# Performance work log

Measured on AMD Instinct MI355X. Metric: run time of the kernel, lower is better.

The kernel has to match this reference:

```python
import jax, jax.numpy as jnp
import numpy as np

N_DRUG, N_TARGET, N_EDGES, H = 50000, 20000, 500000, 256


def setup_inputs() -> dict:
    key = jax.random.key(0)
    ks = jax.random.split(key, 6)
    s = 1.0 / np.sqrt(2 * H)
    return {
        "z_drug": jax.random.normal(ks[0], (N_DRUG, H), dtype=jnp.float32),
        "z_target": jax.random.normal(ks[1], (N_TARGET, H), dtype=jnp.float32),
        "row": jax.random.randint(ks[2], (N_EDGES,), 0, N_DRUG, dtype=jnp.int64),
        "col": jax.random.randint(ks[3], (N_EDGES,), 0, N_TARGET, dtype=jnp.int64),
        "W1": jax.random.normal(ks[4], (2 * H, H), dtype=jnp.float32) * s,
        "b1": jnp.zeros((H,), dtype=jnp.float32),
        "W2": jax.random.normal(ks[5], (H, 1), dtype=jnp.float32) * (1.0 / np.sqrt(H)),
        "b2": jnp.zeros((1,), dtype=jnp.float32),
    }


def reference(z_drug, z_target, row, col, W1, b1, W2, b2):
    # gather endpoint embeddings by edge index, concat -> [E, 2H]
    zc = jnp.concatenate([z_drug[row], z_target[col]], axis=-1)
    h = jax.nn.relu(zc @ W1 + b1)          # [E, H]
    return h @ W2 + b2                     # [E, 1]
```

## Files before the change

kernel.cpp:

```cpp
#include <hip/hip_runtime.h>
#include <hip/hip_bf16.h>
#include <stdint.h>


typedef unsigned short u16;
typedef __attribute__((ext_vector_type(8))) short short8;
typedef __attribute__((ext_vector_type(4))) float f32x4;

#define HDIM 256
#define KDIM 512
#define BM 128
#define BK 64
#define NWAVE 4

__device__ __forceinline__ u16 f2bf(float f) {
  union { float f; uint32_t u; } v; v.f = f;
  uint32_t u = v.u;
  return (u16)((u + 0x7fffu + ((u >> 16) & 1u)) >> 16);
}

__device__ __forceinline__ void gl2lds16(const void* g, void* l) {
  __builtin_amdgcn_global_load_lds(
      (const __attribute__((address_space(1))) unsigned int*)g,
      (__attribute__((address_space(3))) unsigned int*)l,
      16, 0, 0);
}

#define CVT_BLOCKS 4096
__global__ void prep_kernel(const float* __restrict__ zd_f,
                            const float* __restrict__ zt_f,
                            const float* __restrict__ w1,
                            u16* __restrict__ zdb, u16* __restrict__ ztb,
                            u16* __restrict__ w1t, int n4d, int n4t) {
  const int b = blockIdx.x;
  if (b < 32) {
    __shared__ float tile[64][65];
    const int k0 = (b >> 2) * 64, n0 = (b & 3) * 64;
    const int tx = threadIdx.x & 63, ty = threadIdx.x >> 6;
#pragma unroll
    for (int i = ty; i < 64; i += 4)
      tile[i][tx] = w1[(size_t)(k0 + i) * HDIM + n0 + tx];
    __syncthreads();
#pragma unroll
    for (int i = ty; i < 64; i += 4)
      w1t[(size_t)(n0 + i) * KDIM + k0 + tx] = f2bf(tile[tx][i]);
  } else {
    const int idx = (b - 32) * 256 + threadIdx.x;
    const int stride = CVT_BLOCKS * 256;
    for (int i = idx; i < n4d; i += stride) {
      float4 v = ((const float4*)zd_f)[i];
      ushort4 o; o.x = f2bf(v.x); o.y = f2bf(v.y); o.z = f2bf(v.z); o.w = f2bf(v.w);
      ((ushort4*)zdb)[i] = o;
    }
    for (int i = idx; i < n4t; i += stride) {
      float4 v = ((const float4*)zt_f)[i];
      ushort4 o; o.x = f2bf(v.x); o.y = f2bf(v.y); o.z = f2bf(v.z); o.w = f2bf(v.w);
      ((ushort4*)ztb)[i] = o;
    }
  }
}

__global__ __launch_bounds__(256, 2) void edge_mlp_kernel(
    const u16* __restrict__ zd, const u16* __restrict__ zt,
    const int* __restrict__ row, const int* __restrict__ col,
    const u16* __restrict__ w1t, const float* __restrict__ b1,
    const float* __restrict__ w2, const float* __restrict__ b2,
    float* __restrict__ out, int E) {
  __shared__ u16 lA[BM * BK];
  __shared__ u16 lB[HDIM * BK];
  __shared__ float lP[NWAVE * BM];

  const int tid  = threadIdx.x;
  const int wid  = tid >> 6;
  const int lane = tid & 63;
  const int e0   = blockIdx.x * BM;
  const int r8   = lane >> 3;
  const int slog = ((lane & 7) ^ (r8 & 7)) * 8;

  uint32_t offD[4], offT[4];
#pragma unroll
  for (int t = 0; t < 4; ++t) {
    int ge = min(e0 + wid * 32 + r8 + 8 * t, E - 1);
    offD[t] = (uint32_t)row[ge] * HDIM;
    offT[t] = (uint32_t)col[ge] * HDIM;
  }
  const u16* pB = w1t + (uint32_t)(wid * 64 + r8) * KDIM + slog;

  u16* lAw = &lA[(wid * 32) * BK];
  u16* lBw = &lB[(wid * 64) * BK];

  f32x4 acc[8][4];
#pragma unroll
  for (int i = 0; i < 8; ++i)
#pragma unroll
    for (int j = 0; j < 4; ++j) acc[i][j] = f32x4{0.f, 0.f, 0.f, 0.f};

  const int colid = lane & 15;
  const int quad  = lane >> 4;
  const int csw   = colid & 7;

  for (int kc = 0; kc < 8; ++kc) {
    const int koff = (kc & 3) * BK;
    const u16* zbase = (kc < 4) ? zd : zt;

    __syncthreads();
#pragma unroll
    for (int t = 0; t < 4; ++t) {
      uint32_t o = (kc < 4) ? offD[t] : offT[t];
      gl2lds16(zbase + o + koff + slog, lAw + (8 * t) * BK);
    }
#pragma unroll
    for (int j = 0; j < 8; ++j)
      gl2lds16(pB + (size_t)j * 8 * KDIM + kc * BK, lBw + j * 8 * BK);
    __syncthreads();

#pragma unroll
    for (int ks = 0; ks < BK; ks += 32) {
      const int sl = (ks >> 3) + quad;
      short8 aF[8], bF[4];
#pragma unroll
      for (int rt = 0; rt < 8; ++rt)
        aF[rt] = *(const short8*)&lA[(rt * 16 + colid) * BK + ((sl ^ csw) * 8)];
#pragma unroll
      for (int ct = 0; ct < 4; ++ct)
        bF[ct] = *(const short8*)&lB[(wid * 64 + ct * 16 + colid) * BK + ((sl ^ csw) * 8)];
#pragma unroll
      for (int rt = 0; rt < 8; ++rt)
#pragma unroll
        for (int ct = 0; ct < 4; ++ct)
          acc[rt][ct] = __builtin_amdgcn_mfma_f32_16x16x32_bf16(
              aF[rt], bF[ct], acc[rt][ct], 0, 0, 0);
    }
  }

  float b1v[4], w2v[4];
#pragma unroll
  for (int ct = 0; ct < 4; ++ct) {
    int n = wid * 64 + ct * 16 + colid;
    b1v[ct] = b1[n];
    w2v[ct] = w2[n];
  }
#pragma unroll
  for (int rt = 0; rt < 8; ++rt)
#pragma unroll
    for (int j = 0; j < 4; ++j) {
      float s = 0.f;
#pragma unroll
      for (int ct = 0; ct < 4; ++ct)
        s += fmaxf(acc[rt][ct][j] + b1v[ct], 0.f) * w2v[ct];
#pragma unroll
      for (int off = 8; off >= 1; off >>= 1)
        s += __shfl_xor(s, off, 16);
      if (colid == 0)
        lP[wid * BM + rt * 16 + quad * 4 + j] = s;
    }
  __syncthreads();
  if (tid < BM) {
    int ge = e0 + tid;
    if (ge < E)
      out[ge] = lP[tid] + lP[BM + tid] + lP[2 * BM + tid] + lP[3 * BM + tid]
                + b2[0];
  }
}

__global__ void fallback_kernel(
    const float* __restrict__ zd, const float* __restrict__ zt,
    const int* __restrict__ row, const int* __restrict__ col,
    const float* __restrict__ W1, const float* __restrict__ b1,
    const float* __restrict__ W2, const float* __restrict__ b2,
    float* __restrict__ out, int E) {
  __shared__ float zc[16][512];
  __shared__ float red[4][16];
  const int e0 = blockIdx.x * 16;
  const int tid = threadIdx.x;
  for (int i = tid; i < 16 * 512; i += 256) {
    int e = i >> 9, k = i & 511;
    int ge = min(e0 + e, E - 1);
    zc[e][k] = (k < HDIM) ? zd[(size_t)row[ge] * HDIM + k]
                          : zt[(size_t)col[ge] * HDIM + (k - HDIM)];
  }
  __syncthreads();
  float acc[16];
#pragma unroll
  for (int e = 0; e < 16; ++e) acc[e] = 0.f;
  for (int k = 0; k < KDIM; ++k) {
    float w = W1[k * HDIM + tid];
#pragma unroll
    for (int e = 0; e < 16; ++e) acc[e] += zc[e][k] * w;
  }
  float wv = W2[tid], bv = b1[tid];
  const int lane = tid & 63, wid = tid >> 6;
#pragma unroll
  for (int e = 0; e < 16; ++e) {
    float pv = fmaxf(acc[e] + bv, 0.f) * wv;
#pragma unroll
    for (int off = 32; off >= 1; off >>= 1) pv += __shfl_down(pv, off, 64);
    if (lane == 0) red[wid][e] = pv;
  }
  __syncthreads();
  if (tid < 16) {
    int ge = e0 + tid;
    if (ge < E)
      out[ge] = red[0][tid] + red[1][tid] + red[2][tid] + red[3][tid] + b2[0];
  }
}

extern "C" void kernel_launch(void* const* d_in, const int* in_sizes, int n_in,
                              void* d_out, int out_size, void* d_ws, size_t ws_size,
                              hipStream_t stream) {
  const float* zd_f = (const float*)d_in[0];
  const float* zt_f = (const float*)d_in[1];
  const int*   row  = (const int*)d_in[2];
  const int*   col  = (const int*)d_in[3];
  const float* W1   = (const float*)d_in[4];
  const float* b1   = (const float*)d_in[5];
  const float* W2   = (const float*)d_in[6];
  const float* b2   = (const float*)d_in[7];
  float* out = (float*)d_out;

  const int E  = in_sizes[2];
  const int ND = in_sizes[0] / HDIM;
  const int NT = in_sizes[1] / HDIM;

  size_t off_w1t = 0;
  size_t off_zd  = (size_t)KDIM * HDIM * sizeof(u16);
  size_t off_zt  = off_zd + (size_t)ND * HDIM * sizeof(u16);
  size_t need    = off_zt + (size_t)NT * HDIM * sizeof(u16);

  if (ws_size >= need) {
    u16* w1t = (u16*)((char*)d_ws + off_w1t);
    u16* zdb = (u16*)((char*)d_ws + off_zd);
    u16* ztb = (u16*)((char*)d_ws + off_zt);
    int n4d = ND * HDIM / 4, n4t = NT * HDIM / 4;
    prep_kernel<<<32 + CVT_BLOCKS, 256, 0, stream>>>(zd_f, zt_f, W1,
                                                     zdb, ztb, w1t, n4d, n4t);
    edge_mlp_kernel<<<(E + BM - 1) / BM, 256, 0, stream>>>(
        zdb, ztb, row, col, w1t, b1, W2, b2, out, E);
  } else {
    fallback_kernel<<<(E + 15) / 16, 256, 0, stream>>>(
        zd_f, zt_f, row, col, W1, b1, W2, b2, out, E);
  }
}
```

Before: 268.1 us.

## Load A fragments directly to registers and double-buffer W1 tiles in LDS

Each wave now owns 32 edges across all 256 hidden outputs instead of 128 edges by 64 outputs. The gathered embedding rows are read straight from global memory into MFMA register fragments, prefetched one K-chunk ahead. W1 tiles are double-buffered in LDS so the next chunk's load overlaps the current MFMAs, cutting one barrier per iteration. The final reduction no longer goes through LDS; the cost is more W1 reads per edge from LDS and direct global gathers that bypass LDS.

```diff
diff --git a/kernel.cpp b/kernel.cpp
--- a/kernel.cpp
+++ b/kernel.cpp
@@ -11,7 +11,7 @@
 #define KDIM 512
 #define BM 128
 #define BK 64
-#define NWAVE 4
+#define NKC 8
 
 __device__ __forceinline__ u16 f2bf(float f) {
   union { float f; uint32_t u; } v; v.f = f;
@@ -66,101 +66,105 @@
     const u16* __restrict__ w1t, const float* __restrict__ b1,
     const float* __restrict__ w2, const float* __restrict__ b2,
     float* __restrict__ out, int E) {
-  __shared__ u16 lA[BM * BK];
-  __shared__ u16 lB[HDIM * BK];
-  __shared__ float lP[NWAVE * BM];
-
-  const int tid  = threadIdx.x;
-  const int wid  = tid >> 6;
-  const int lane = tid & 63;
-  const int e0   = blockIdx.x * BM;
-  const int r8   = lane >> 3;
-  const int slog = ((lane & 7) ^ (r8 & 7)) * 8;
-
-  uint32_t offD[4], offT[4];
-#pragma unroll
-  for (int t = 0; t < 4; ++t) {
-    int ge = min(e0 + wid * 32 + r8 + 8 * t, E - 1);
-    offD[t] = (uint32_t)row[ge] * HDIM;
-    offT[t] = (uint32_t)col[ge] * HDIM;
-  }
-  const u16* pB = w1t + (uint32_t)(wid * 64 + r8) * KDIM + slog;
-
-  u16* lAw = &lA[(wid * 32) * BK];
-  u16* lBw = &lB[(wid * 64) * BK];
-
-  f32x4 acc[8][4];
-#pragma unroll
-  for (int i = 0; i < 8; ++i)
-#pragma unroll
-    for (int j = 0; j < 4; ++j) acc[i][j] = f32x4{0.f, 0.f, 0.f, 0.f};
-
+  __shared__ u16 lB[2][HDIM * BK];
+
+  const int tid   = threadIdx.x;
+  const int wid   = tid >> 6;
+  const int lane  = tid & 63;
   const int colid = lane & 15;
   const int quad  = lane >> 4;
+  const int e0    = blockIdx.x * BM;
+  const int r8    = lane >> 3;
+  const int slog  = ((lane & 7) ^ (r8 & 7)) * 8;
   const int csw   = colid & 7;
 
-  for (int kc = 0; kc < 8; ++kc) {
-    const int koff = (kc & 3) * BK;
-    const u16* zbase = (kc < 4) ? zd : zt;
-
-    __syncthreads();
-#pragma unroll
-    for (int t = 0; t < 4; ++t) {
-      uint32_t o = (kc < 4) ? offD[t] : offT[t];
-      gl2lds16(zbase + o + koff + slog, lAw + (8 * t) * BK);
-    }
-#pragma unroll
-    for (int j = 0; j < 8; ++j)
-      gl2lds16(pB + (size_t)j * 8 * KDIM + kc * BK, lBw + j * 8 * BK);
-    __syncthreads();
-
-#pragma unroll
-    for (int ks = 0; ks < BK; ks += 32) {
-      const int sl = (ks >> 3) + quad;
-      short8 aF[8], bF[4];
-#pragma unroll
-      for (int rt = 0; rt < 8; ++rt)
-        aF[rt] = *(const short8*)&lA[(rt * 16 + colid) * BK + ((sl ^ csw) * 8)];
-#pragma unroll
-      for (int ct = 0; ct < 4; ++ct)
-        bF[ct] = *(const short8*)&lB[(wid * 64 + ct * 16 + colid) * BK + ((sl ^ csw) * 8)];
-#pragma unroll
-      for (int rt = 0; rt < 8; ++rt)
-#pragma unroll
-        for (int ct = 0; ct < 4; ++ct)
-          acc[rt][ct] = __builtin_amdgcn_mfma_f32_16x16x32_bf16(
-              aF[rt], bF[ct], acc[rt][ct], 0, 0, 0);
-    }
-  }
-
-  float b1v[4], w2v[4];
-#pragma unroll
-  for (int ct = 0; ct < 4; ++ct) {
-    int n = wid * 64 + ct * 16 + colid;
-    b1v[ct] = b1[n];
-    w2v[ct] = w2[n];
-  }
-#pragma unroll
-  for (int rt = 0; rt < 8; ++rt)
+  const u16* aB[2][2];
+#pragma unroll
+  for (int rt = 0; rt < 2; ++rt) {
+    int ge = min(e0 + wid * 32 + rt * 16 + colid, E - 1);
+    aB[rt][0] = zd + (size_t)row[ge] * HDIM;
+    aB[rt][1] = zt + (size_t)col[ge] * HDIM;
+  }
+  const u16* pB = w1t + (size_t)(wid * 64 + r8) * KDIM + slog;
+
+  f32x4 acc[2][16];
+#pragma unroll
+  for (int rt = 0; rt < 2; ++rt)
+#pragma unroll
+    for (int ct = 0; ct < 16; ++ct) acc[rt][ct] = f32x4{0.f, 0.f, 0.f, 0.f};
+
+  short8 aCur[2][2], aNxt[2][2];
+
+#pragma unroll
+  for (int rt = 0; rt < 2; ++rt)
+#pragma unroll
+    for (int h = 0; h < 2; ++h)
+      aCur[rt][h] = *(const short8*)(aB[rt][0] + (quad + 4 * h) * 8);
+#pragma unroll
+  for (int j = 0; j < 8; ++j)
+    gl2lds16(pB + (size_t)j * 8 * KDIM, &lB[0][(wid * 64 + j * 8) * BK]);
+  __syncthreads();
+
+#pragma unroll
+  for (int kc = 0; kc < NKC; ++kc) {
+    if (kc + 1 < NKC) {
+      const int kn = kc + 1;
+#pragma unroll
+      for (int rt = 0; rt < 2; ++rt)
+#pragma unroll
+        for (int h = 0; h < 2; ++h)
+          aNxt[rt][h] = *(const short8*)(aB[rt][kn >> 2] + (kn & 3) * BK +
+                                         (quad + 4 * h) * 8);
+#pragma unroll
+      for (int j = 0; j < 8; ++j)
+        gl2lds16(pB + (size_t)j * 8 * KDIM + kn * BK,
+                 &lB[kn & 1][(wid * 64 + j * 8) * BK]);
+    }
+
+    const u16* lb = lB[kc & 1];
+#pragma unroll
+    for (int h = 0; h < 2; ++h) {
+      const int sl = quad + 4 * h;
+#pragma unroll
+      for (int ct = 0; ct < 16; ++ct) {
+        short8 bF = *(const short8*)&lb[(ct * 16 + colid) * BK +
+                                        ((sl ^ csw) * 8)];
+        acc[0][ct] = __builtin_amdgcn_mfma_f32_16x16x32_bf16(
+            aCur[0][h], bF, acc[0][ct], 0, 0, 0);
+        acc[1][ct] = __builtin_amdgcn_mfma_f32_16x16x32_bf16(
+            aCur[1][h], bF, acc[1][ct], 0, 0, 0);
+      }
+    }
+#pragma unroll
+    for (int rt = 0; rt < 2; ++rt)
+#pragma unroll
+      for (int h = 0; h < 2; ++h) aCur[rt][h] = aNxt[rt][h];
+    if (kc + 1 < NKC) __syncthreads();
+  }
+
+  float b1v[16], w2v[16];
+#pragma unroll
+  for (int ct = 0; ct < 16; ++ct) {
+    b1v[ct] = b1[ct * 16 + colid];
+    w2v[ct] = w2[ct * 16 + colid];
+  }
+  const float bias2 = b2[0];
+#pragma unroll
+  for (int rt = 0; rt < 2; ++rt)
 #pragma unroll
     for (int j = 0; j < 4; ++j) {
       float s = 0.f;
 #pragma unroll
-      for (int ct = 0; ct < 4; ++ct)
+      for (int ct = 0; ct < 16; ++ct)
         s += fmaxf(acc[rt][ct][j] + b1v[ct], 0.f) * w2v[ct];
 #pragma unroll
       for (int off = 8; off >= 1; off >>= 1)
         s += __shfl_xor(s, off, 16);
-      if (colid == 0)
-        lP[wid * BM + rt * 16 + quad * 4 + j] = s;
-    }
-  __syncthreads();
-  if (tid < BM) {
-    int ge = e0 + tid;
-    if (ge < E)
-      out[ge] = lP[tid] + lP[BM + tid] + lP[2 * BM + tid] + lP[3 * BM + tid]
-                + b2[0];
-  }
+      if (colid == 0) {
+        int ge = e0 + wid * 32 + rt * 16 + quad * 4 + j;
+        if (ge < E) out[ge] = s + bias2;
+      }
+    }
 }
 
 __global__ void fallback_kernel(
```

Result: no change. 270.3 us (+0.8%).

## Load MFMA operands directly from global into registers with double buffering

Applied to the files above, without the earlier changes.

Drops the LDS staging of the gathered A rows and W1 tiles. Each lane now loads its MFMA fragments straight from global memory into registers, prefetching the next K-chunk while the current one computes. The edge tile shrinks from 128 to 64 rows per block so the register double-buffers fit. This removes LDS traffic and block barriers, but every wave now reloads W1 from L2 with no sharing through LDS, and the 16-byte per-lane gathers are less coalesced.

```diff
diff --git a/kernel.cpp b/kernel.cpp
--- a/kernel.cpp
+++ b/kernel.cpp
@@ -9,21 +9,14 @@
 
 #define HDIM 256
 #define KDIM 512
-#define BM 128
+#define BM 64
 #define BK 64
-#define NWAVE 4
+#define NKC 8
 
 __device__ __forceinline__ u16 f2bf(float f) {
   union { float f; uint32_t u; } v; v.f = f;
   uint32_t u = v.u;
   return (u16)((u + 0x7fffu + ((u >> 16) & 1u)) >> 16);
-}
-
-__device__ __forceinline__ void gl2lds16(const void* g, void* l) {
-  __builtin_amdgcn_global_load_lds(
-      (const __attribute__((address_space(1))) unsigned int*)g,
-      (__attribute__((address_space(3))) unsigned int*)l,
-      16, 0, 0);
 }
 
 #define CVT_BLOCKS 4096
@@ -66,71 +59,75 @@
     const u16* __restrict__ w1t, const float* __restrict__ b1,
     const float* __restrict__ w2, const float* __restrict__ b2,
     float* __restrict__ out, int E) {
-  __shared__ u16 lA[BM * BK];
-  __shared__ u16 lB[HDIM * BK];
-  __shared__ float lP[NWAVE * BM];
-
-  const int tid  = threadIdx.x;
-  const int wid  = tid >> 6;
-  const int lane = tid & 63;
-  const int e0   = blockIdx.x * BM;
-  const int r8   = lane >> 3;
-  const int slog = ((lane & 7) ^ (r8 & 7)) * 8;
-
-  uint32_t offD[4], offT[4];
-#pragma unroll
-  for (int t = 0; t < 4; ++t) {
-    int ge = min(e0 + wid * 32 + r8 + 8 * t, E - 1);
-    offD[t] = (uint32_t)row[ge] * HDIM;
-    offT[t] = (uint32_t)col[ge] * HDIM;
-  }
-  const u16* pB = w1t + (uint32_t)(wid * 64 + r8) * KDIM + slog;
-
-  u16* lAw = &lA[(wid * 32) * BK];
-  u16* lBw = &lB[(wid * 64) * BK];
-
-  f32x4 acc[8][4];
-#pragma unroll
-  for (int i = 0; i < 8; ++i)
-#pragma unroll
-    for (int j = 0; j < 4; ++j) acc[i][j] = f32x4{0.f, 0.f, 0.f, 0.f};
-
+  __shared__ float lP[4][BM];
+
+  const int tid   = threadIdx.x;
+  const int wid   = tid >> 6;
+  const int lane  = tid & 63;
   const int colid = lane & 15;
   const int quad  = lane >> 4;
-  const int csw   = colid & 7;
-
-  for (int kc = 0; kc < 8; ++kc) {
-    const int koff = (kc & 3) * BK;
-    const u16* zbase = (kc < 4) ? zd : zt;
-
-    __syncthreads();
-#pragma unroll
-    for (int t = 0; t < 4; ++t) {
-      uint32_t o = (kc < 4) ? offD[t] : offT[t];
-      gl2lds16(zbase + o + koff + slog, lAw + (8 * t) * BK);
-    }
-#pragma unroll
-    for (int j = 0; j < 8; ++j)
-      gl2lds16(pB + (size_t)j * 8 * KDIM + kc * BK, lBw + j * 8 * BK);
-    __syncthreads();
-
-#pragma unroll
-    for (int ks = 0; ks < BK; ks += 32) {
-      const int sl = (ks >> 3) + quad;
-      short8 aF[8], bF[4];
-#pragma unroll
-      for (int rt = 0; rt < 8; ++rt)
-        aF[rt] = *(const short8*)&lA[(rt * 16 + colid) * BK + ((sl ^ csw) * 8)];
+  const int e0    = blockIdx.x * BM;
+
+  uint32_t offD[4], offT[4];
+#pragma unroll
+  for (int rt = 0; rt < 4; ++rt) {
+    int ge = min(e0 + rt * 16 + colid, E - 1);
+    offD[rt] = (uint32_t)row[ge] * HDIM;
+    offT[rt] = (uint32_t)col[ge] * HDIM;
+  }
+  const u16* bBase = w1t + (size_t)(wid * 64 + colid) * KDIM + quad * 8;
+
+  f32x4 acc[4][4];
+#pragma unroll
+  for (int i = 0; i < 4; ++i)
+#pragma unroll
+    for (int j = 0; j < 4; ++j) acc[i][j] = f32x4{0.f, 0.f, 0.f, 0.f};
+
+  short8 aC[4][2], aN[4][2], bC[4][2], bN[4][2];
+
+#define LOAD_A(kc, dst)                                                        \
+  {                                                                            \
+    const u16* base = ((kc) < 4) ? zd : zt;                                    \
+    const int ko = ((kc) & 3) * BK;                                            \
+    _Pragma("unroll") for (int rt = 0; rt < 4; ++rt) {                         \
+      uint32_t o = ((kc) < 4) ? offD[rt] : offT[rt];                           \
+      _Pragma("unroll") for (int h = 0; h < 2; ++h)                            \
+          dst[rt][h] = *(const short8*)(base + o + ko + h * 32 + quad * 8);    \
+    }                                                                          \
+  }
+
+#define LOAD_B(kc, dst)                                                        \
+  {                                                                            \
+    _Pragma("unroll") for (int ct = 0; ct < 4; ++ct)                           \
+        _Pragma("unroll") for (int h = 0; h < 2; ++h)                          \
+            dst[ct][h] =                                                       \
+        *(const short8*)(bBase + (size_t)(ct * 16) * KDIM + (kc) * BK + h * 32);\
+  }
+
+  LOAD_A(0, aC);
+  LOAD_B(0, bC);
+
+#pragma unroll
+  for (int kc = 0; kc < NKC; ++kc) {
+    if (kc + 1 < NKC) {
+      LOAD_A(kc + 1, aN);
+      LOAD_B(kc + 1, bN);
+    }
+#pragma unroll
+    for (int h = 0; h < 2; ++h)
 #pragma unroll
       for (int ct = 0; ct < 4; ++ct)
-        bF[ct] = *(const short8*)&lB[(wid * 64 + ct * 16 + colid) * BK + ((sl ^ csw) * 8)];
-#pragma unroll
-      for (int rt = 0; rt < 8; ++rt)
-#pragma unroll
-        for (int ct = 0; ct < 4; ++ct)
+#pragma unroll
+        for (int rt = 0; rt < 4; ++rt)
           acc[rt][ct] = __builtin_amdgcn_mfma_f32_16x16x32_bf16(
-              aF[rt], bF[ct], acc[rt][ct], 0, 0, 0);
-    }
+              aC[rt][h], bC[ct][h], acc[rt][ct], 0, 0, 0);
+#pragma unroll
+    for (int rt = 0; rt < 4; ++rt)
+#pragma unroll
+      for (int h = 0; h < 2; ++h) {
+        aC[rt][h] = aN[rt][h];
+        bC[rt][h] = bN[rt][h];
+      }
   }
 
   float b1v[4], w2v[4];
@@ -141,7 +138,7 @@
     w2v[ct] = w2[n];
   }
 #pragma unroll
-  for (int rt = 0; rt < 8; ++rt)
+  for (int rt = 0; rt < 4; ++rt)
 #pragma unroll
     for (int j = 0; j < 4; ++j) {
       float s = 0.f;
@@ -151,15 +148,13 @@
 #pragma unroll
       for (int off = 8; off >= 1; off >>= 1)
         s += __shfl_xor(s, off, 16);
-      if (colid == 0)
-        lP[wid * BM + rt * 16 + quad * 4 + j] = s;
+      if (colid == 0) lP[wid][rt * 16 + quad * 4 + j] = s;
     }
   __syncthreads();
   if (tid < BM) {
     int ge = e0 + tid;
     if (ge < E)
-      out[ge] = lP[tid] + lP[BM + tid] + lP[2 * BM + tid] + lP[3 * BM + tid]
-                + b2[0];
+      out[ge] = lP[0][tid] + lP[1][tid] + lP[2][tid] + lP[3][tid] + b2[0];
   }
 }
 
```

New measurement: 559.6 us. 109% more time.
